# Kernel optimization log

Hardware: AMD Instinct MI355X
Metric: run time of the kernel (lower is better)

Reference implementation:

```python
import jax, jax.numpy as jnp
import numpy as np

N_SITE, D, PHYS, W = 40, 128, 2, 8  # sites, MPS bond dim, physical dim, MPO bond dim


def setup_inputs() -> dict:
    key = jax.random.key(0)
    k1, k2 = jax.random.split(key)
    # scale so 40-step transfer-matrix products stay O(1) in float32
    M = jax.random.normal(k1, (N_SITE, D, PHYS, D), jnp.float32) * (D * PHYS) ** -0.5
    H = jax.random.normal(k2, (N_SITE, W, W, PHYS, PHYS), jnp.float32) * (W * PHYS * PHYS) ** -0.5
    return {"M": M, "H": H}


def _energy(M, H):
    # <M|H|M> via left-to-right environment sweep. L has shape (D_bra, w, D_ket).
    L0 = jnp.zeros((D, W, D), M.dtype).at[0, 0, 0].set(1.0)  # open left boundary

    def step(L, mh):
        m, h = mh  # m: (a,i,p) bond,phys,bond ; h: (w,x,i,j) mpo-bond,mpo-bond,phys-out,phys-in
        T = jnp.einsum('awb,aip->wbip', L, m)      # absorb bra tensor (real, so no conj)
        T = jnp.einsum('wbip,wxij->bpxj', T, h)    # absorb MPO tensor
        L = jnp.einsum('bpxj,bjq->pxq', T, m)      # absorb ket tensor
        return L, None

    L, _ = jax.lax.scan(step, L0, (M, H))
    return L[0, W - 1, 0]  # open right boundary (MPO right boundary = last index)


def _norm(M):
    # <M|M> via transfer-matrix sweep. N has shape (D_bra, D_ket); stays PSD.
    N0 = jnp.zeros((D, D), M.dtype).at[0, 0].set(1.0)

    def step(N, m):
        T = jnp.einsum('ab,aip->bip', N, m)
        N = jnp.einsum('bip,biq->pq', T, m)
        return N, None

    N, _ = jax.lax.scan(step, N0, M)
    return N[0, 0]


def reference(M, H):
    EPS = 0.0
    NORM_LIM = 10000.0
    energy = _energy(M, H)
    norm = _norm(M)
    loss = energy / (norm + EPS)  # torch.real is identity for real dtype
    reg = jax.nn.relu(norm - NORM_LIM)
    return (energy, norm, loss, reg)
```

## Files before the change

kernel.cpp:

```cpp
#include <hip/hip_runtime.h>


#define D 128
#define W 8
#define NS 40
#define NPAIR 20
#define HALF2 10
#define MSZ (D * 2 * D)
#define HSZ (W * W * 2 * 2)
#define M2SZ (D * 4 * D)
#define H2SZ (W * W * 4 * 4)
#define LSZ (D * W * D)
#define NSZ (D * D)
#define T2SZ (D * W * D * 4)
#define TNSZ (4 * D * D)

#define OFF_M2 0
#define OFF_MR2 (OFF_M2 + NPAIR * M2SZ)
#define OFF_H2 (OFF_MR2 + HALF2 * M2SZ)
#define OFF_HR2 (OFF_H2 + NPAIR * H2SZ)
#define OFF_LL (OFF_HR2 + HALF2 * H2SZ)
#define OFF_LR (OFF_LL + LSZ)
#define OFF_NL (OFF_LR + LSZ)
#define OFF_NR (OFF_NL + NSZ)
#define OFF_T2L (OFF_NR + NSZ)
#define OFF_T2R (OFF_T2L + T2SZ)
#define OFF_TNL (OFF_T2R + T2SZ)
#define OFF_TNR (OFF_TNL + TNSZ)
#define OFF_PART (OFF_TNR + TNSZ)
#define OFF_PARTN (OFF_PART + 128)

__global__ __launch_bounds__(256) void k_prep1(const float* __restrict__ Min,
                                               const float* __restrict__ Hin,
                                               float* __restrict__ ws) {
    __shared__ float As[32 * 34];
    __shared__ float Bs[32 * 68];
    int bid = blockIdx.x, t = threadIdx.x;
    if (bid < 640) {
        int m = bid >> 5, tile = bid & 31;
        int r0 = (tile & 7) * 32, c0 = (tile >> 3) * 64;
        const float* A = Min + (2 * m) * MSZ;
        const float* B = Min + (2 * m + 1) * MSZ;
        float* C = ws + OFF_M2 + m * M2SZ;
        int ty = t >> 4, tx = t & 15;
        float a00 = 0, a01 = 0, a02 = 0, a03 = 0;
        float a10 = 0, a11 = 0, a12 = 0, a13 = 0;
        for (int c = 0; c < 4; ++c) {
            int k0 = c * 32;
            __syncthreads();
            {
                int rr = t >> 3, kq = t & 7;
                int row = r0 + rr;
                const float4 v = *(const float4*)&A[(row >> 1) * 256 + (row & 1) * 128 + k0 + kq * 4];
                float* dst = &As[kq * 136 + rr];
                dst[0] = v.x; dst[34] = v.y; dst[68] = v.z; dst[102] = v.w;
            }
#pragma unroll
            for (int u = 0; u < 2; ++u) {
                int e = u * 256 + t;
                int kk = e >> 4, cq = e & 15;
                const float4 v = *(const float4*)&B[(k0 + kk) * 256 + c0 + cq * 4];
                *(float4*)&Bs[kk * 68 + cq * 4] = v;
            }
            __syncthreads();
#pragma unroll 8
            for (int kk = 0; kk < 32; ++kk) {
                float2 av = *(float2*)&As[kk * 34 + 2 * ty];
                float4 bv = *(float4*)&Bs[kk * 68 + 4 * tx];
                a00 += av.x * bv.x; a01 += av.x * bv.y; a02 += av.x * bv.z; a03 += av.x * bv.w;
                a10 += av.y * bv.x; a11 += av.y * bv.y; a12 += av.y * bv.z; a13 += av.y * bv.w;
            }
        }
        int r = r0 + 2 * ty, cc = c0 + 4 * tx;
        int a = r >> 1, i2 = cc >> 7, cd = cc & 127;
        float4 v0; v0.x = a00; v0.y = a01; v0.z = a02; v0.w = a03;
        float4 v1; v1.x = a10; v1.y = a11; v1.z = a12; v1.w = a13;
        *(float4*)&C[a * 512 + (0 * 2 + i2) * 128 + cd] = v0;
        *(float4*)&C[a * 512 + (1 * 2 + i2) * 128 + cd] = v1;
    } else {
        for (int idx = t; idx < NPAIR * H2SZ; idx += 256) {
            int m = idx >> 10, r = idx & 1023;
            int w = r >> 7, x = (r >> 4) & 7, I = (r >> 2) & 3, J = r & 3;
            int i1 = I >> 1, i2 = I & 1, j1 = J >> 1, j2 = J & 1;
            const float* Ha = Hin + (2 * m) * HSZ;
            const float* Hb = Hin + (2 * m + 1) * HSZ;
            float s = 0.f;
#pragma unroll
            for (int v = 0; v < 8; ++v)
                s += Ha[w * 32 + v * 4 + i1 * 2 + j1] * Hb[v * 32 + x * 4 + i2 * 2 + j2];
            ws[OFF_H2 + idx] = s;
        }
    }
}

#define PR_MR (HALF2 * M2SZ)
#define PR_HR (PR_MR + HALF2 * H2SZ)
#define PR_TOT (PR_HR + 2 * LSZ + 2 * NSZ)
__global__ __launch_bounds__(256) void k_prep2(float* __restrict__ ws) {
    for (int idx = blockIdx.x * 256 + threadIdx.x; idx < PR_TOT; idx += gridDim.x * 256) {
        if (idx < PR_MR) {
            int kr = idx >> 16, r = idx & 65535;
            int a = r >> 9, I = (r >> 7) & 3, p = r & 127;
            ws[OFF_MR2 + idx] = ws[OFF_M2 + (19 - kr) * M2SZ + p * 512 + I * 128 + a];
        } else if (idx < PR_HR) {
            int e = idx - PR_MR;
            int kr = e >> 10, r = e & 1023;
            int w = r >> 7, x = (r >> 4) & 7, lo = r & 15;
            ws[OFF_HR2 + e] = ws[OFF_H2 + (19 - kr) * H2SZ + x * 128 + w * 16 + lo];
        } else {
            int e = idx - PR_HR;
            int off; float v = 0.f;
            if (e < LSZ)            { off = OFF_LL + e; if (e == 0) v = 1.f; }
            else if (e < 2 * LSZ)   { int r = e - LSZ; off = OFF_LR + r; if (r == (W - 1) * D) v = 1.f; }
            else if (e < 2 * LSZ + NSZ) { int r = e - 2 * LSZ; off = OFF_NL + r; if (r == 0) v = 1.f; }
            else                    { int r = e - 2 * LSZ - NSZ; off = OFF_NR + r; if (r == 0) v = 1.f; }
            ws[off] = v;
        }
    }
}

__global__ __launch_bounds__(256) void k_A2(const float* __restrict__ ws_c,
                                            float* __restrict__ ws, int k) {
    __shared__ float sm[9472];
    (void)ws_c;
    int bid = blockIdx.x, t = threadIdx.x;
    if (bid < 128) {
        int side = bid >> 6;
        int eb = bid & 63;
        int b0 = (eb & 7) * 16;
        int p0 = (eb >> 3) * 16;
        const float* Lsrc = ws + (side ? OFF_LR : OFF_LL);
        const float* m2 = ws + (side ? OFF_MR2 : OFF_M2) + k * M2SZ;
        const float* h2 = ws + (side ? OFF_HR2 : OFF_H2) + k * H2SZ;
        float* T2 = ws + (side ? OFF_T2R : OFF_T2L);
        float* Ls = sm;
        float* ms = sm + 6400;
        float* hs = sm + 8448;
#pragma unroll
        for (int u = 0; u < 4; ++u) {
            int e = u * 256 + t;
            int w = e >> 7, I = (e >> 5) & 3, x = (e >> 2) & 7, J = e & 3;
            hs[e] = h2[w * 128 + x * 16 + I * 4 + J];
        }
        int b_l = t & 15, p_l = t >> 4;
        float acc[8][4];
#pragma unroll
        for (int w = 0; w < 8; ++w)
#pragma unroll
            for (int I = 0; I < 4; ++I) acc[w][I] = 0.f;
        for (int c = 0; c < 4; ++c) {
            int a0 = c * 32;
            __syncthreads();
#pragma unroll
            for (int u = 0; u < 4; ++u) {
                int e = u * 256 + t;
                int aa = e >> 5, w = (e >> 2) & 7, bq = e & 3;
                const float4 v = *(const float4*)&Lsrc[(a0 + aa) * 1024 + w * 128 + b0 + bq * 4];
                float* dst = &Ls[aa * 200 + bq * 48 + w];
                dst[0] = v.x; dst[12] = v.y; dst[24] = v.z; dst[36] = v.w;
            }
#pragma unroll
            for (int u = 0; u < 2; ++u) {
                int s = u * 256 + t;
                int aa = s >> 4, I = (s >> 2) & 3, pq = s & 3;
                const float4 v = *(const float4*)&m2[(a0 + aa) * 512 + I * 128 + p0 + pq * 4];
                *(float4*)&ms[aa * 64 + I * 16 + pq * 4] = v;
            }
            __syncthreads();
#pragma unroll 4
            for (int aa = 0; aa < 32; ++aa) {
                float4 l0 = *(float4*)&Ls[aa * 200 + b_l * 12];
                float4 l1 = *(float4*)&Ls[aa * 200 + b_l * 12 + 4];
                float lw[8] = {l0.x, l0.y, l0.z, l0.w, l1.x, l1.y, l1.z, l1.w};
                float mv[4];
#pragma unroll
                for (int I = 0; I < 4; ++I) mv[I] = ms[aa * 64 + I * 16 + p_l];
#pragma unroll
                for (int w = 0; w < 8; ++w)
#pragma unroll
                    for (int I = 0; I < 4; ++I) acc[w][I] += lw[w] * mv[I];
            }
        }
        float o[32];
#pragma unroll
        for (int xJ = 0; xJ < 32; ++xJ) o[xJ] = 0.f;
#pragma unroll
        for (int wI = 0; wI < 32; ++wI) {
            float tv = acc[wI >> 2][wI & 3];
#pragma unroll
            for (int xJ = 0; xJ < 32; ++xJ) o[xJ] += tv * hs[wI * 32 + xJ];
        }
        int b = b0 + b_l, p = p0 + p_l;
#pragma unroll
        for (int x = 0; x < 8; ++x) {
            float4 v; v.x = o[x * 4]; v.y = o[x * 4 + 1]; v.z = o[x * 4 + 2]; v.w = o[x * 4 + 3];
            *(float4*)&T2[p * 4096 + x * 512 + b * 4] = v;
        }
    } else {
        int nb = bid - 128;
        int side = nb >> 5;
        int nn = nb & 31;
        int b0 = (nn & 3) * 32;
        int c0 = (nn >> 2) * 64;
        const float* Nsrc = ws + (side ? OFF_NR : OFF_NL);
        const float* m2 = ws + (side ? OFF_MR2 : OFF_M2) + k * M2SZ;
        float* Tn = ws + (side ? OFF_TNR : OFF_TNL);
        float* As = sm;
        float* Bs = sm + 1056;
        int ty = t >> 4, tx = t & 15;
        float a00 = 0, a01 = 0, a02 = 0, a03 = 0;
        float a10 = 0, a11 = 0, a12 = 0, a13 = 0;
        for (int c = 0; c < 4; ++c) {
            int a0 = c * 32;
            __syncthreads();
#pragma unroll
            for (int u = 0; u < 4; ++u) {
                int e = u * 256 + t;
                int kk = e >> 5, col = e & 31;
                As[kk * 33 + col] = Nsrc[(a0 + kk) * 128 + b0 + col];
            }
#pragma unroll
            for (int u = 0; u < 8; ++u) {
                int e = u * 256 + t;
                int kk = e >> 6, col = e & 63;
                Bs[kk * 68 + col] = m2[(a0 + kk) * 512 + c0 + col];
            }
            __syncthreads();
#pragma unroll 8
            for (int kk = 0; kk < 32; ++kk) {
                float2 av = *(float2*)&As[kk * 33 + 2 * ty];
                float4 bv = *(float4*)&Bs[kk * 68 + 4 * tx];
                a00 += av.x * bv.x; a01 += av.x * bv.y; a02 += av.x * bv.z; a03 += av.x * bv.w;
                a10 += av.y * bv.x; a11 += av.y * bv.y; a12 += av.y * bv.z; a13 += av.y * bv.w;
            }
        }
        int b_ = b0 + 2 * ty;
        float rowv[2][4] = {{a00, a01, a02, a03}, {a10, a11, a12, a13}};
#pragma unroll
        for (int jj = 0; jj < 4; ++jj) {
            int col = c0 + 4 * tx + jj;
            int I = col >> 7, p = col & 127;
            Tn[I * 16384 + p * 128 + b_] = rowv[0][jj];
            Tn[I * 16384 + p * 128 + b_ + 1] = rowv[1][jj];
        }
    }
}

__global__ __launch_bounds__(256) void k_B2(float* __restrict__ ws, int k) {
    __shared__ float As[32 * 34];
    __shared__ float Bs[32 * 68];
    int bid = blockIdx.x, t = threadIdx.x;
    int ty = t >> 4, tx = t & 15;
    float a00 = 0, a01 = 0, a02 = 0, a03 = 0;
    float a10 = 0, a11 = 0, a12 = 0, a13 = 0;
    if (bid < 128) {
        int side = bid >> 6;
        int eb = bid & 63;
        int r0 = (eb & 31) * 32;
        int c0 = (eb >> 5) * 64;
        const float* A = ws + (side ? OFF_T2R : OFF_T2L);
        const float* B = ws + (side ? OFF_MR2 : OFF_M2) + k * M2SZ;
        float* C = ws + (side ? OFF_LR : OFF_LL);
        for (int c = 0; c < 16; ++c) {
            int k0 = c * 32;
            __syncthreads();
            {
                int rr = t >> 3, kq = t & 7;
                const float4 v = *(const float4*)&A[(r0 + rr) * 512 + k0 + kq * 4];
                float* dst = &As[kq * 136 + rr];
                dst[0] = v.x; dst[34] = v.y; dst[68] = v.z; dst[102] = v.w;
            }
#pragma unroll
            for (int u = 0; u < 2; ++u) {
                int e = u * 256 + t;
                int kk = e >> 4, cq = e & 15;
                int row = k0 + kk;
                const float4 v = *(const float4*)&B[(row >> 2) * 512 + (row & 3) * 128 + c0 + cq * 4];
                *(float4*)&Bs[kk * 68 + cq * 4] = v;
            }
            __syncthreads();
#pragma unroll 8
            for (int kk = 0; kk < 32; ++kk) {
                float2 av = *(float2*)&As[kk * 34 + 2 * ty];
                float4 bv = *(float4*)&Bs[kk * 68 + 4 * tx];
                a00 += av.x * bv.x; a01 += av.x * bv.y; a02 += av.x * bv.z; a03 += av.x * bv.w;
                a10 += av.y * bv.x; a11 += av.y * bv.y; a12 += av.y * bv.z; a13 += av.y * bv.w;
            }
        }
        int r = r0 + 2 * ty, cc = c0 + 4 * tx;
        float4 v0; v0.x = a00; v0.y = a01; v0.z = a02; v0.w = a03;
        float4 v1; v1.x = a10; v1.y = a11; v1.z = a12; v1.w = a13;
        *(float4*)&C[(r >> 3) * 1024 + (r & 7) * 128 + cc] = v0;
        *(float4*)&C[((r + 1) >> 3) * 1024 + ((r + 1) & 7) * 128 + cc] = v1;
    } else if (bid < 144) {
        int nb = bid - 128;
        int side = nb >> 3;
        int nn = nb & 7;
        int r0 = (nn & 3) * 32;
        int c0 = (nn >> 2) * 64;
        const float* A = ws + (side ? OFF_TNR : OFF_TNL);
        const float* B = ws + (side ? OFF_MR2 : OFF_M2) + k * M2SZ;
        float* C = ws + (side ? OFF_NR : OFF_NL);
        for (int c = 0; c < 16; ++c) {
            int k0 = c * 32;
            int Ic = k0 >> 7, bc = k0 & 127;
            __syncthreads();
            {
                int rr = t >> 3, kq = t & 7;
                const float4 v = *(const float4*)&A[Ic * 16384 + (r0 + rr) * 128 + bc + kq * 4];
                float* dst = &As[kq * 136 + rr];
                dst[0] = v.x; dst[34] = v.y; dst[68] = v.z; dst[102] = v.w;
            }
#pragma unroll
            for (int u = 0; u < 2; ++u) {
                int e = u * 256 + t;
                int kk = e >> 4, cq = e & 15;
                const float4 v = *(const float4*)&B[(bc + kk) * 512 + Ic * 128 + c0 + cq * 4];
                *(float4*)&Bs[kk * 68 + cq * 4] = v;
            }
            __syncthreads();
#pragma unroll 8
            for (int kk = 0; kk < 32; ++kk) {
                float2 av = *(float2*)&As[kk * 34 + 2 * ty];
                float4 bv = *(float4*)&Bs[kk * 68 + 4 * tx];
                a00 += av.x * bv.x; a01 += av.x * bv.y; a02 += av.x * bv.z; a03 += av.x * bv.w;
                a10 += av.y * bv.x; a11 += av.y * bv.y; a12 += av.y * bv.z; a13 += av.y * bv.w;
            }
        }
        int r = r0 + 2 * ty, cc = c0 + 4 * tx;
        float4 v0; v0.x = a00; v0.y = a01; v0.z = a02; v0.w = a03;
        float4 v1; v1.x = a10; v1.y = a11; v1.z = a12; v1.w = a13;
        *(float4*)&C[r * 128 + cc] = v0;
        *(float4*)&C[(r + 1) * 128 + cc] = v1;
    }
}

__global__ __launch_bounds__(256) void k_dot(float* __restrict__ ws) {
    __shared__ float se[256], sn[256];
    int bid = blockIdx.x, t = threadIdx.x;
    const float* LL = ws + OFF_LL;
    const float* LR = ws + OFF_LR;
    float e = 0.f;
#pragma unroll
    for (int u = 0; u < 4; ++u) {
        int i = bid * 1024 + u * 256 + t;
        e += LL[i] * LR[i];
    }
    float n = 0.f;
    if (t < 128) {
        int i = bid * 128 + t;
        n = ws[OFF_NL + i] * ws[OFF_NR + i];
    }
    se[t] = e;
    sn[t] = n;
    __syncthreads();
    for (int s = 128; s > 0; s >>= 1) {
        if (t < s) { se[t] += se[t + s]; sn[t] += sn[t + s]; }
        __syncthreads();
    }
    if (t == 0) {
        ws[OFF_PART + bid] = se[0];
        ws[OFF_PARTN + bid] = sn[0];
    }
}

__global__ __launch_bounds__(256) void k_loss(const float* __restrict__ ws,
                                              float* __restrict__ out) {
    __shared__ float se[128], sn[128];
    int t = threadIdx.x;
    if (t < 128) {
        se[t] = ws[OFF_PART + t];
        sn[t] = ws[OFF_PARTN + t];
    }
    __syncthreads();
    for (int s = 64; s > 0; s >>= 1) {
        if (t < s) { se[t] += se[t + s]; sn[t] += sn[t + s]; }
        __syncthreads();
    }
    if (t == 0) {
        float E = se[0], Nm = sn[0];
        out[0] = E;
        out[1] = Nm;
        out[2] = E / Nm;
        out[3] = fmaxf(Nm - 10000.0f, 0.0f);
    }
}

extern "C" void kernel_launch(void* const* d_in, const int* in_sizes, int n_in,
                              void* d_out, int out_size, void* d_ws, size_t ws_size,
                              hipStream_t stream) {
    const float* Min = (const float*)d_in[0];
    const float* Hin = (const float*)d_in[1];
    float* ws = (float*)d_ws;
    float* out = (float*)d_out;
    (void)in_sizes; (void)n_in; (void)out_size; (void)ws_size;

    k_prep1<<<dim3(641), dim3(256), 0, stream>>>(Min, Hin, ws);
    k_prep2<<<dim3(640), dim3(256), 0, stream>>>(ws);
    for (int k = 0; k < HALF2; ++k) {
        k_A2<<<dim3(192), dim3(256), 0, stream>>>(ws, ws, k);
        k_B2<<<dim3(144), dim3(256), 0, stream>>>(ws, k);
    }
    k_dot<<<dim3(128), dim3(256), 0, stream>>>(ws);
    k_loss<<<dim3(1), dim3(256), 0, stream>>>(ws, out);
}
```

Before: 476.8 us.

## Split reduction dimension across two thread halves with register prefetch in A2/B2

Blocks grow to 512 threads. In k_A2 the I dimension is split between the two halves, and partial outputs are summed through shared memory. In k_B2 the K dimension is split and reduced through shared memory, and the norm-path blocks in k_A2 are packed two per block. Global loads are also prefetched into registers one tile ahead to overlap with compute. The aim is more parallelism per block on a latency-bound sequential sweep, at the cost of extra syncs, shared-memory reduction traffic and register pressure.

```diff
diff --git a/kernel.cpp b/kernel.cpp
--- a/kernel.cpp
+++ b/kernel.cpp
@@ -119,11 +119,10 @@
     }
 }
 
-__global__ __launch_bounds__(256) void k_A2(const float* __restrict__ ws_c,
-                                            float* __restrict__ ws, int k) {
-    __shared__ float sm[9472];
-    (void)ws_c;
+__global__ __launch_bounds__(512) void k_A2(float* __restrict__ ws, int k) {
+    __shared__ __align__(16) float sm[9472];
     int bid = blockIdx.x, t = threadIdx.x;
+    int z = t >> 8, tl = t & 255;
     if (bid < 128) {
         int side = bid >> 6;
         int eb = bid & 63;
@@ -137,34 +136,36 @@
         float* ms = sm + 6400;
         float* hs = sm + 8448;
 #pragma unroll
-        for (int u = 0; u < 4; ++u) {
-            int e = u * 256 + t;
+        for (int u = 0; u < 2; ++u) {
+            int e = u * 512 + t;
             int w = e >> 7, I = (e >> 5) & 3, x = (e >> 2) & 7, J = e & 3;
             hs[e] = h2[w * 128 + x * 16 + I * 4 + J];
         }
-        int b_l = t & 15, p_l = t >> 4;
-        float acc[8][4];
-#pragma unroll
-        for (int w = 0; w < 8; ++w)
-#pragma unroll
-            for (int I = 0; I < 4; ++I) acc[w][I] = 0.f;
+        int b_l = tl & 15, p_l = tl >> 4;
+        float acc[8][2];
+#pragma unroll
+        for (int w = 0; w < 8; ++w) { acc[w][0] = 0.f; acc[w][1] = 0.f; }
+        int e0 = t, e1 = 512 + t;
+        int la0 = e0 >> 5, lw0 = (e0 >> 2) & 7, lb0 = e0 & 3;
+        int la1 = e1 >> 5, lw1 = (e1 >> 2) & 7, lb1 = e1 & 3;
+        int maa = t >> 4, mI = (t >> 2) & 3, mpq = t & 3;
+        float4 pl0 = *(const float4*)&Lsrc[la0 * 1024 + lw0 * 128 + b0 + lb0 * 4];
+        float4 pl1 = *(const float4*)&Lsrc[la1 * 1024 + lw1 * 128 + b0 + lb1 * 4];
+        float4 pm = *(const float4*)&m2[maa * 512 + mI * 128 + p0 + mpq * 4];
         for (int c = 0; c < 4; ++c) {
-            int a0 = c * 32;
-            __syncthreads();
-#pragma unroll
-            for (int u = 0; u < 4; ++u) {
-                int e = u * 256 + t;
-                int aa = e >> 5, w = (e >> 2) & 7, bq = e & 3;
-                const float4 v = *(const float4*)&Lsrc[(a0 + aa) * 1024 + w * 128 + b0 + bq * 4];
-                float* dst = &Ls[aa * 200 + bq * 48 + w];
-                dst[0] = v.x; dst[12] = v.y; dst[24] = v.z; dst[36] = v.w;
-            }
-#pragma unroll
-            for (int u = 0; u < 2; ++u) {
-                int s = u * 256 + t;
-                int aa = s >> 4, I = (s >> 2) & 3, pq = s & 3;
-                const float4 v = *(const float4*)&m2[(a0 + aa) * 512 + I * 128 + p0 + pq * 4];
-                *(float4*)&ms[aa * 64 + I * 16 + pq * 4] = v;
+            __syncthreads();
+            {
+                float* d0 = &Ls[la0 * 200 + lb0 * 48 + lw0];
+                d0[0] = pl0.x; d0[12] = pl0.y; d0[24] = pl0.z; d0[36] = pl0.w;
+                float* d1 = &Ls[la1 * 200 + lb1 * 48 + lw1];
+                d1[0] = pl1.x; d1[12] = pl1.y; d1[24] = pl1.z; d1[36] = pl1.w;
+                *(float4*)&ms[maa * 64 + mI * 16 + mpq * 4] = pm;
+            }
+            if (c < 3) {
+                int a0 = (c + 1) * 32;
+                pl0 = *(const float4*)&Lsrc[(a0 + la0) * 1024 + lw0 * 128 + b0 + lb0 * 4];
+                pl1 = *(const float4*)&Lsrc[(a0 + la1) * 1024 + lw1 * 128 + b0 + lb1 * 4];
+                pm = *(const float4*)&m2[(a0 + maa) * 512 + mI * 128 + p0 + mpq * 4];
             }
             __syncthreads();
 #pragma unroll 4
@@ -172,42 +173,60 @@
                 float4 l0 = *(float4*)&Ls[aa * 200 + b_l * 12];
                 float4 l1 = *(float4*)&Ls[aa * 200 + b_l * 12 + 4];
                 float lw[8] = {l0.x, l0.y, l0.z, l0.w, l1.x, l1.y, l1.z, l1.w};
-                float mv[4];
-#pragma unroll
-                for (int I = 0; I < 4; ++I) mv[I] = ms[aa * 64 + I * 16 + p_l];
-#pragma unroll
-                for (int w = 0; w < 8; ++w)
-#pragma unroll
-                    for (int I = 0; I < 4; ++I) acc[w][I] += lw[w] * mv[I];
+                float mv0 = ms[aa * 64 + (2 * z) * 16 + p_l];
+                float mv1 = ms[aa * 64 + (2 * z + 1) * 16 + p_l];
+#pragma unroll
+                for (int w = 0; w < 8; ++w) {
+                    acc[w][0] += lw[w] * mv0;
+                    acc[w][1] += lw[w] * mv1;
+                }
             }
         }
         float o[32];
 #pragma unroll
         for (int xJ = 0; xJ < 32; ++xJ) o[xJ] = 0.f;
 #pragma unroll
-        for (int wI = 0; wI < 32; ++wI) {
-            float tv = acc[wI >> 2][wI & 3];
-#pragma unroll
-            for (int xJ = 0; xJ < 32; ++xJ) o[xJ] += tv * hs[wI * 32 + xJ];
-        }
-        int b = b0 + b_l, p = p0 + p_l;
-#pragma unroll
-        for (int x = 0; x < 8; ++x) {
-            float4 v; v.x = o[x * 4]; v.y = o[x * 4 + 1]; v.z = o[x * 4 + 2]; v.w = o[x * 4 + 3];
-            *(float4*)&T2[p * 4096 + x * 512 + b * 4] = v;
+        for (int w = 0; w < 8; ++w)
+#pragma unroll
+            for (int ii = 0; ii < 2; ++ii) {
+                float tv = acc[w][ii];
+                int wI = w * 4 + 2 * z + ii;
+#pragma unroll
+                for (int xJ = 0; xJ < 32; ++xJ) o[xJ] += tv * hs[wI * 32 + xJ];
+            }
+        __syncthreads();
+        if (z == 1) {
+#pragma unroll
+            for (int j = 0; j < 8; ++j) {
+                float4 v; v.x = o[j * 4]; v.y = o[j * 4 + 1];
+                v.z = o[j * 4 + 2]; v.w = o[j * 4 + 3];
+                *(float4*)&sm[tl * 32 + j * 4] = v;
+            }
+        }
+        __syncthreads();
+        if (z == 0) {
+#pragma unroll
+            for (int j = 0; j < 32; ++j) o[j] += sm[tl * 32 + j];
+            int b = b0 + b_l, p = p0 + p_l;
+#pragma unroll
+            for (int x = 0; x < 8; ++x) {
+                float4 v; v.x = o[x * 4]; v.y = o[x * 4 + 1];
+                v.z = o[x * 4 + 2]; v.w = o[x * 4 + 3];
+                *(float4*)&T2[p * 4096 + x * 512 + b * 4] = v;
+            }
         }
     } else {
-        int nb = bid - 128;
-        int side = nb >> 5;
-        int nn = nb & 31;
+        int g = (bid - 128) * 2 + z;
+        int side = g >> 5;
+        int nn = g & 31;
         int b0 = (nn & 3) * 32;
         int c0 = (nn >> 2) * 64;
         const float* Nsrc = ws + (side ? OFF_NR : OFF_NL);
         const float* m2 = ws + (side ? OFF_MR2 : OFF_M2) + k * M2SZ;
         float* Tn = ws + (side ? OFF_TNR : OFF_TNL);
-        float* As = sm;
-        float* Bs = sm + 1056;
-        int ty = t >> 4, tx = t & 15;
+        float* As = sm + z * 3264;
+        float* Bs = sm + z * 3264 + 1056;
+        int ty = tl >> 4, tx = tl & 15;
         float a00 = 0, a01 = 0, a02 = 0, a03 = 0;
         float a10 = 0, a11 = 0, a12 = 0, a13 = 0;
         for (int c = 0; c < 4; ++c) {
@@ -215,23 +234,23 @@
             __syncthreads();
 #pragma unroll
             for (int u = 0; u < 4; ++u) {
-                int e = u * 256 + t;
+                int e = u * 256 + tl;
                 int kk = e >> 5, col = e & 31;
                 As[kk * 33 + col] = Nsrc[(a0 + kk) * 128 + b0 + col];
             }
 #pragma unroll
             for (int u = 0; u < 8; ++u) {
-                int e = u * 256 + t;
+                int e = u * 256 + tl;
                 int kk = e >> 6, col = e & 63;
                 Bs[kk * 68 + col] = m2[(a0 + kk) * 512 + c0 + col];
             }
             __syncthreads();
 #pragma unroll 8
             for (int kk = 0; kk < 32; ++kk) {
-                float2 av = *(float2*)&As[kk * 33 + 2 * ty];
+                float av0 = As[kk * 33 + 2 * ty], av1 = As[kk * 33 + 2 * ty + 1];
                 float4 bv = *(float4*)&Bs[kk * 68 + 4 * tx];
-                a00 += av.x * bv.x; a01 += av.x * bv.y; a02 += av.x * bv.z; a03 += av.x * bv.w;
-                a10 += av.y * bv.x; a11 += av.y * bv.y; a12 += av.y * bv.z; a13 += av.y * bv.w;
+                a00 += av0 * bv.x; a01 += av0 * bv.y; a02 += av0 * bv.z; a03 += av0 * bv.w;
+                a10 += av1 * bv.x; a11 += av1 * bv.y; a12 += av1 * bv.z; a13 += av1 * bv.w;
             }
         }
         int b_ = b0 + 2 * ty;
@@ -246,13 +265,16 @@
     }
 }
 
-__global__ __launch_bounds__(256) void k_B2(float* __restrict__ ws, int k) {
-    __shared__ float As[32 * 34];
-    __shared__ float Bs[32 * 68];
+__global__ __launch_bounds__(512) void k_B2(float* __restrict__ ws, int k) {
+    __shared__ __align__(16) float sm[8576];
     int bid = blockIdx.x, t = threadIdx.x;
-    int ty = t >> 4, tx = t & 15;
+    int z = t >> 8, tl = t & 255;
+    int ty = tl >> 4, tx = tl & 15;
     float a00 = 0, a01 = 0, a02 = 0, a03 = 0;
     float a10 = 0, a11 = 0, a12 = 0, a13 = 0;
+    float* As = sm + z * 3264;
+    float* Bs = sm + z * 3264 + 1088;
+    float* red = sm + 6528;
     if (bid < 128) {
         int side = bid >> 6;
         int eb = bid & 63;
@@ -261,59 +283,79 @@
         const float* A = ws + (side ? OFF_T2R : OFF_T2L);
         const float* B = ws + (side ? OFF_MR2 : OFF_M2) + k * M2SZ;
         float* C = ws + (side ? OFF_LR : OFF_LL);
-        for (int c = 0; c < 16; ++c) {
-            int k0 = c * 32;
+        int rr = tl >> 3, kq = tl & 7;
+        int kkb0 = tl >> 4, cq0 = tl & 15;
+        int kkb1 = (256 + tl) >> 4, cq1 = tl & 15;
+        int k0 = (z * 8) * 32;
+        float4 pa = *(const float4*)&A[(r0 + rr) * 512 + k0 + kq * 4];
+        int row0 = k0 + kkb0, row1 = k0 + kkb1;
+        float4 pb0 = *(const float4*)&B[(row0 >> 2) * 512 + (row0 & 3) * 128 + c0 + cq0 * 4];
+        float4 pb1 = *(const float4*)&B[(row1 >> 2) * 512 + (row1 & 3) * 128 + c0 + cq1 * 4];
+        for (int c = 0; c < 8; ++c) {
             __syncthreads();
             {
-                int rr = t >> 3, kq = t & 7;
-                const float4 v = *(const float4*)&A[(r0 + rr) * 512 + k0 + kq * 4];
                 float* dst = &As[kq * 136 + rr];
-                dst[0] = v.x; dst[34] = v.y; dst[68] = v.z; dst[102] = v.w;
-            }
-#pragma unroll
-            for (int u = 0; u < 2; ++u) {
-                int e = u * 256 + t;
-                int kk = e >> 4, cq = e & 15;
-                int row = k0 + kk;
-                const float4 v = *(const float4*)&B[(row >> 2) * 512 + (row & 3) * 128 + c0 + cq * 4];
-                *(float4*)&Bs[kk * 68 + cq * 4] = v;
+                dst[0] = pa.x; dst[34] = pa.y; dst[68] = pa.z; dst[102] = pa.w;
+                *(float4*)&Bs[kkb0 * 68 + cq0 * 4] = pb0;
+                *(float4*)&Bs[kkb1 * 68 + cq1 * 4] = pb1;
+            }
+            if (c < 7) {
+                int kn = (z * 8 + c + 1) * 32;
+                pa = *(const float4*)&A[(r0 + rr) * 512 + kn + kq * 4];
+                int r0n = kn + kkb0, r1n = kn + kkb1;
+                pb0 = *(const float4*)&B[(r0n >> 2) * 512 + (r0n & 3) * 128 + c0 + cq0 * 4];
+                pb1 = *(const float4*)&B[(r1n >> 2) * 512 + (r1n & 3) * 128 + c0 + cq1 * 4];
             }
             __syncthreads();
 #pragma unroll 8
             for (int kk = 0; kk < 32; ++kk) {
-                float2 av = *(float2*)&As[kk * 34 + 2 * ty];
+                float av0 = As[kk * 34 + 2 * ty], av1 = As[kk * 34 + 2 * ty + 1];
                 float4 bv = *(float4*)&Bs[kk * 68 + 4 * tx];
-                a00 += av.x * bv.x; a01 += av.x * bv.y; a02 += av.x * bv.z; a03 += av.x * bv.w;
-                a10 += av.y * bv.x; a11 += av.y * bv.y; a12 += av.y * bv.z; a13 += av.y * bv.w;
-            }
-        }
-        int r = r0 + 2 * ty, cc = c0 + 4 * tx;
-        float4 v0; v0.x = a00; v0.y = a01; v0.z = a02; v0.w = a03;
-        float4 v1; v1.x = a10; v1.y = a11; v1.z = a12; v1.w = a13;
-        *(float4*)&C[(r >> 3) * 1024 + (r & 7) * 128 + cc] = v0;
-        *(float4*)&C[((r + 1) >> 3) * 1024 + ((r + 1) & 7) * 128 + cc] = v1;
+                a00 += av0 * bv.x; a01 += av0 * bv.y; a02 += av0 * bv.z; a03 += av0 * bv.w;
+                a10 += av1 * bv.x; a11 += av1 * bv.y; a12 += av1 * bv.z; a13 += av1 * bv.w;
+            }
+        }
+        __syncthreads();
+        if (z == 1) {
+            float4 v0; v0.x = a00; v0.y = a01; v0.z = a02; v0.w = a03;
+            float4 v1; v1.x = a10; v1.y = a11; v1.z = a12; v1.w = a13;
+            *(float4*)&red[tl * 8] = v0;
+            *(float4*)&red[tl * 8 + 4] = v1;
+        }
+        __syncthreads();
+        if (z == 0) {
+            float4 v0 = *(float4*)&red[tl * 8];
+            float4 v1 = *(float4*)&red[tl * 8 + 4];
+            a00 += v0.x; a01 += v0.y; a02 += v0.z; a03 += v0.w;
+            a10 += v1.x; a11 += v1.y; a12 += v1.z; a13 += v1.w;
+            int r = r0 + 2 * ty, cc = c0 + 4 * tx;
+            float4 w0; w0.x = a00; w0.y = a01; w0.z = a02; w0.w = a03;
+            float4 w1; w1.x = a10; w1.y = a11; w1.z = a12; w1.w = a13;
+            *(float4*)&C[(r >> 3) * 1024 + (r & 7) * 128 + cc] = w0;
+            *(float4*)&C[((r + 1) >> 3) * 1024 + ((r + 1) & 7) * 128 + cc] = w1;
+        }
     } else if (bid < 144) {
-        int nb = bid - 128;
-        int side = nb >> 3;
-        int nn = nb & 7;
+        int g = bid - 128;
+        int side = g >> 3;
+        int nn = g & 7;
         int r0 = (nn & 3) * 32;
         int c0 = (nn >> 2) * 64;
         const float* A = ws + (side ? OFF_TNR : OFF_TNL);
         const float* B = ws + (side ? OFF_MR2 : OFF_M2) + k * M2SZ;
         float* C = ws + (side ? OFF_NR : OFF_NL);
-        for (int c = 0; c < 16; ++c) {
-            int k0 = c * 32;
-            int Ic = k0 >> 7, bc = k0 & 127;
+        for (int c = 0; c < 8; ++c) {
+            int cg = z * 8 + c;
+            int Ic = cg >> 2, bc = (cg & 3) * 32;
             __syncthreads();
             {
-                int rr = t >> 3, kq = t & 7;
+                int rr = tl >> 3, kq = tl & 7;
                 const float4 v = *(const float4*)&A[Ic * 16384 + (r0 + rr) * 128 + bc + kq * 4];
                 float* dst = &As[kq * 136 + rr];
                 dst[0] = v.x; dst[34] = v.y; dst[68] = v.z; dst[102] = v.w;
             }
 #pragma unroll
             for (int u = 0; u < 2; ++u) {
-                int e = u * 256 + t;
+                int e = u * 256 + tl;
                 int kk = e >> 4, cq = e & 15;
                 const float4 v = *(const float4*)&B[(bc + kk) * 512 + Ic * 128 + c0 + cq * 4];
                 *(float4*)&Bs[kk * 68 + cq * 4] = v;
@@ -321,17 +363,31 @@
             __syncthreads();
 #pragma unroll 8
             for (int kk = 0; kk < 32; ++kk) {
-                float2 av = *(float2*)&As[kk * 34 + 2 * ty];
+                float av0 = As[kk * 34 + 2 * ty], av1 = As[kk * 34 + 2 * ty + 1];
                 float4 bv = *(float4*)&Bs[kk * 68 + 4 * tx];
-                a00 += av.x * bv.x; a01 += av.x * bv.y; a02 += av.x * bv.z; a03 += av.x * bv.w;
-                a10 += av.y * bv.x; a11 += av.y * bv.y; a12 += av.y * bv.z; a13 += av.y * bv.w;
-            }
-        }
-        int r = r0 + 2 * ty, cc = c0 + 4 * tx;
-        float4 v0; v0.x = a00; v0.y = a01; v0.z = a02; v0.w = a03;
-        float4 v1; v1.x = a10; v1.y = a11; v1.z = a12; v1.w = a13;
-        *(float4*)&C[r * 128 + cc] = v0;
-        *(float4*)&C[(r + 1) * 128 + cc] = v1;
+                a00 += av0 * bv.x; a01 += av0 * bv.y; a02 += av0 * bv.z; a03 += av0 * bv.w;
+                a10 += av1 * bv.x; a11 += av1 * bv.y; a12 += av1 * bv.z; a13 += av1 * bv.w;
+            }
+        }
+        __syncthreads();
+        if (z == 1) {
+            float4 v0; v0.x = a00; v0.y = a01; v0.z = a02; v0.w = a03;
+            float4 v1; v1.x = a10; v1.y = a11; v1.z = a12; v1.w = a13;
+            *(float4*)&red[tl * 8] = v0;
+            *(float4*)&red[tl * 8 + 4] = v1;
+        }
+        __syncthreads();
+        if (z == 0) {
+            float4 v0 = *(float4*)&red[tl * 8];
+            float4 v1 = *(float4*)&red[tl * 8 + 4];
+            a00 += v0.x; a01 += v0.y; a02 += v0.z; a03 += v0.w;
+            a10 += v1.x; a11 += v1.y; a12 += v1.z; a13 += v1.w;
+            int r = r0 + 2 * ty, cc = c0 + 4 * tx;
+            float4 w0; w0.x = a00; w0.y = a01; w0.z = a02; w0.w = a03;
+            float4 w1; w1.x = a10; w1.y = a11; w1.z = a12; w1.w = a13;
+            *(float4*)&C[r * 128 + cc] = w0;
+            *(float4*)&C[(r + 1) * 128 + cc] = w1;
+        }
     }
 }
 
@@ -398,8 +454,8 @@
     k_prep1<<<dim3(641), dim3(256), 0, stream>>>(Min, Hin, ws);
     k_prep2<<<dim3(640), dim3(256), 0, stream>>>(ws);
     for (int k = 0; k < HALF2; ++k) {
-        k_A2<<<dim3(192), dim3(256), 0, stream>>>(ws, ws, k);
-        k_B2<<<dim3(144), dim3(256), 0, stream>>>(ws, k);
+        k_A2<<<dim3(160), dim3(512), 0, stream>>>(ws, k);
+        k_B2<<<dim3(144), dim3(512), 0, stream>>>(ws, k);
     }
     k_dot<<<dim3(128), dim3(256), 0, stream>>>(ws);
     k_loss<<<dim3(1), dim3(256), 0, stream>>>(ws, out);
```

Result: faster. 385.9 us (-19.1%).
